# Kernel optimization log

Hardware: AMD Instinct MI355X
Metric: run time of the kernel (lower is better)

The kernel has to match this reference:

```python
import math
import jax, jax.numpy as jnp
import numpy as np

N_HEADS = 12


def _rel_to_abs(x):
    # x: [b, h, L, 2L-1] relative logits -> [b, h, L, L] absolute-position scores
    b, h, L, _ = x.shape
    x = jnp.pad(x, ((0, 0), (0, 0), (0, 0), (0, 1)))           # [b,h,L,2L]
    xf = x.reshape(b, h, L * 2 * L)
    xf = jnp.pad(xf, ((0, 0), (0, 0), (0, L - 1)))
    return xf.reshape(b, h, L + 1, 2 * L - 1)[:, :, :L, L - 1:]


def _abs_to_rel(x):
    # x: [b, h, L, L] attention weights -> [b, h, L, 2L-1] relative-position weights
    b, h, L, _ = x.shape
    x = jnp.pad(x, ((0, 0), (0, 0), (0, 0), (0, L - 1)))        # [b,h,L,2L-1]
    xf = x.reshape(b, h, L * (2 * L - 1))
    xf = jnp.pad(xf, ((0, 0), (0, 0), (L, 0)))
    return xf.reshape(b, h, L, 2 * L)[:, :, :, 1:]


def _get_relative_embeddings(emb, length):
    # emb: [n_rel, 2*window+1, k] -> [n_rel, 2*length-1, k]
    window = (emb.shape[1] - 1) // 2
    pad_len = max(length - (window + 1), 0)
    start = max(window + 1 - length, 0)
    if pad_len > 0:
        emb = jnp.pad(emb, ((0, 0), (pad_len, pad_len), (0, 0)))
    return emb[:, start:start + 2 * length - 1]


def setup_inputs() -> dict:
    key = jax.random.key(0)
    ks = jax.random.split(key, 8)
    B, C, T, H = 4, 768, 1024, N_HEADS
    K = C // H
    W = 10
    xavier = math.sqrt(2.0 / (C + C))          # xavier_uniform std analogue
    rel_std = K ** (-0.5)
    return {
        "x": jax.random.normal(ks[0], (B, C, T), jnp.float32),
        "c": jax.random.normal(ks[1], (B, C, T), jnp.float32),
        "Wq": jax.random.normal(ks[2], (C, C), jnp.float32) * xavier,
        "bq": jnp.zeros((C,), jnp.float32),
        "Wk": jax.random.normal(ks[3], (C, C), jnp.float32) * xavier,
        "bk": jnp.zeros((C,), jnp.float32),
        "Wv": jax.random.normal(ks[4], (C, C), jnp.float32) * xavier,
        "bv": jnp.zeros((C,), jnp.float32),
        "Wo": jax.random.normal(ks[5], (C, C), jnp.float32) * xavier,
        "bo": jnp.zeros((C,), jnp.float32),
        "emb_rel_k": jax.random.normal(ks[6], (1, 2 * W + 1, K), jnp.float32) * rel_std,
        "emb_rel_v": jax.random.normal(ks[7], (1, 2 * W + 1, K), jnp.float32) * rel_std,
    }


def reference(x, c, Wq, bq, Wk, bk, Wv, bv, Wo, bo, emb_rel_k, emb_rel_v):
    B, C, T = x.shape
    H = N_HEADS
    K = C // H

    def proj(W_, b_, inp):  # Conv1d(kernel=1) == channel-wise linear
        return jnp.einsum('oi,bit->bot', W_, inp) + b_[None, :, None]

    # [B,C,T] -> [B,H,T,K]
    q = proj(Wq, bq, x).reshape(B, H, K, T).transpose(0, 1, 3, 2)
    k = proj(Wk, bk, c).reshape(B, H, K, T).transpose(0, 1, 3, 2)
    v = proj(Wv, bv, c).reshape(B, H, K, T).transpose(0, 1, 3, 2)

    qs = q * (1.0 / math.sqrt(K))
    scores = jnp.einsum('bhtd,bhsd->bhts', qs, k)               # [B,H,T,T]

    # relative key logits via skewing trick
    rel_k = _get_relative_embeddings(emb_rel_k, T)              # [1,2T-1,K]
    rel_logits = jnp.einsum('bhtd,md->bhtm', qs, rel_k[0])      # [B,H,T,2T-1]
    scores = scores + _rel_to_abs(rel_logits)

    # proximal bias: -log(1 + |i - j|)
    r = jnp.arange(T, dtype=scores.dtype)
    scores = scores - jnp.log1p(jnp.abs(r[None, :] - r[:, None]))[None, None]

    p = jax.nn.softmax(scores, axis=-1)
    out = jnp.einsum('bhts,bhsd->bhtd', p, v)                   # [B,H,T,K]

    # relative value contribution
    rel_v = _get_relative_embeddings(emb_rel_v, T)              # [1,2T-1,K]
    out = out + jnp.einsum('bhtm,md->bhtd', _abs_to_rel(p), rel_v[0])

    out = out.transpose(0, 1, 3, 2).reshape(B, C, T)            # [B,C,T]
    return jnp.einsum('oi,bit->bot', Wo, out) + bo[None, :, None]
```

## Files before the change

kernel.cpp:

```cpp
#include <hip/hip_runtime.h>
#include <hip/hip_bf16.h>

using bf16 = __hip_bfloat16;
typedef __attribute__((ext_vector_type(8))) short short8;
typedef __attribute__((ext_vector_type(4))) float f32x4;

static constexpr int C = 768, T = 1024, H = 12, D = 64;

__device__ __forceinline__ f32x4 mfma16(short8 a, short8 b, f32x4 c){
  return __builtin_amdgcn_mfma_f32_16x16x32_bf16(a, b, c, 0, 0, 0);
}

__device__ __forceinline__ void gload16(const void* g, void* l){
  void* gv = const_cast<void*>(g);
  __builtin_amdgcn_global_load_lds((__attribute__((address_space(1))) void*)gv,
                                   (__attribute__((address_space(3))) void*)l, 16, 0, 0);
}

__device__ __forceinline__ float b2f(short s){
  unsigned u = ((unsigned)(unsigned short)s) << 16;
  return __builtin_bit_cast(float, u);
}

__device__ __forceinline__ int cvtpk(float a, float b){
  int r;
  asm("v_cvt_pk_bf16_f32 %0, %1, %2" : "=v"(r) : "v"(a), "v"(b));
  return r;
}

union PkU { int i[4]; short8 v; };

__global__ __launch_bounds__(256) void prep_kernel(const float* __restrict__ xin,
    const float* __restrict__ cin, const float* __restrict__ Wq,
    const float* __restrict__ Wk, const float* __restrict__ Wv,
    const float* __restrict__ Wo, bf16* __restrict__ xo, bf16* __restrict__ co,
    bf16* __restrict__ wq, bf16* __restrict__ wk, bf16* __restrict__ wv,
    bf16* __restrict__ wo){
  const int z = blockIdx.z;
  if (z < 8){
    __shared__ float tile[64][65];
    const int b = z & 3, which = z >> 2;
    const float* in = which ? cin : xin;
    bf16* out = which ? co : xo;
    const int t0 = blockIdx.x*64, c0 = blockIdx.y*64;
    const int u = threadIdx.x & 63, r0 = threadIdx.x >> 6;
    const float* ip = in + ((size_t)b*C + c0)*T + t0;
    #pragma unroll
    for (int i = r0; i < 64; i += 4) tile[i][u] = ip[(size_t)i*T + u];
    __syncthreads();
    bf16* op = out + ((size_t)b*T + t0)*C + c0;
    #pragma unroll
    for (int j = r0; j < 64; j += 4) op[(size_t)j*C + u] = (bf16)tile[u][j];
  } else {
    const int chunk = (z - 8)*192 + blockIdx.y*16 + blockIdx.x;
    const int m = chunk / 576;
    const int off = (chunk % 576)*1024 + threadIdx.x*4;
    const float* in = m==0 ? Wq : m==1 ? Wk : m==2 ? Wv : Wo;
    bf16* out = m==0 ? wq : m==1 ? wk : m==2 ? wv : wo;
    float4 v = *(const float4*)(in + off);
    out[off+0] = (bf16)v.x; out[off+1] = (bf16)v.y;
    out[off+2] = (bf16)v.z; out[off+3] = (bf16)v.w;
  }
}

__global__ __launch_bounds__(256,3) void gemm_qkv(const bf16* __restrict__ xb,
    const bf16* __restrict__ cb, const bf16* __restrict__ wq, const bf16* __restrict__ wk,
    const bf16* __restrict__ wv, const float* __restrict__ bq, const float* __restrict__ bk,
    const float* __restrict__ bv, bf16* __restrict__ qout, bf16* __restrict__ kout,
    bf16* __restrict__ vout){
  const int tid = threadIdx.x, lane = tid & 63, w = tid >> 6;
  const int wr = w >> 1, wc = w & 1, g = lane >> 4, cl = lane & 15;
  const int bz = blockIdx.y, b = bz & 3, mode = bz >> 2;
  const int lb = blockIdx.x;
  int m0, n0;
  if (mode == 2){ m0 = (lb >> 3)*128; n0 = (lb & 7)*128; }
  else          { m0 = (lb / 6)*128;  n0 = (lb % 6)*128; }
  const bf16* A  = (mode==0) ? xb + (size_t)b*T*C : (mode==1) ? cb + (size_t)b*T*C : wv;
  const bf16* Bp = (mode==2) ? cb + (size_t)b*T*C : (mode==0) ? wq : wk;
  const float* bias = (mode==0) ? bq : (mode==1) ? bk : bv;
  const float scale = (mode==0) ? 0.125f*1.44269504088896f : 1.0f;
  __shared__ bf16 lA[128*64], lB[128*64];
  f32x4 acc[4][4] = {};
  const bf16* Ars = A  + (size_t)m0*768;
  const bf16* Brs = Bp + (size_t)n0*768;
  for (int k0 = 0; k0 < 768; k0 += 64){
    __syncthreads();
    #pragma unroll
    for (int rr = 0; rr < 4; ++rr){
      const int u = rr*256 + tid;
      const int row = u >> 3, cc = u & 7;
      const int src = row*768 + k0 + ((cc ^ (row & 7))*8);
      gload16(Ars + src, &lA[(size_t)u*8]);
      gload16(Brs + src, &lB[(size_t)u*8]);
    }
    __syncthreads();
    #pragma unroll
    for (int kh = 0; kh < 2; ++kh){
      short8 af[4], bfr[4];
      #pragma unroll
      for (int mi = 0; mi < 4; ++mi){
        const int row = wr*64 + mi*16 + cl;
        af[mi] = *(const short8*)&lA[row*64 + (((g + kh*4) ^ (row & 7))*8)];
      }
      #pragma unroll
      for (int ni = 0; ni < 4; ++ni){
        const int row = wc*64 + ni*16 + cl;
        bfr[ni] = *(const short8*)&lB[row*64 + (((g + kh*4) ^ (row & 7))*8)];
      }
      __builtin_amdgcn_s_setprio(1);
      #pragma unroll
      for (int mi = 0; mi < 4; ++mi)
        #pragma unroll
        for (int ni = 0; ni < 4; ++ni)
          acc[mi][ni] = mfma16(af[mi], bfr[ni], acc[mi][ni]);
      __builtin_amdgcn_s_setprio(0);
    }
  }
  #pragma unroll
  for (int mi = 0; mi < 4; ++mi){
    const int mB = m0 + wr*64 + mi*16 + g*4;
    #pragma unroll
    for (int ni = 0; ni < 4; ++ni){
      const int n = n0 + wc*64 + ni*16 + cl;
      #pragma unroll
      for (int r = 0; r < 4; ++r){
        const int m = mB + r;
        float v = acc[mi][ni][r];
        if (mode <= 1){
          v = (v + bias[n]) * scale;
          bf16* outp = mode ? kout : qout;
          outp[(size_t)b*(H*T*D) + (size_t)(n >> 6)*(T*D) + (size_t)m*D + (n & 63)] = (bf16)v;
        } else {
          v += bias[m];
          vout[(size_t)b*(C*T) + (size_t)m*T + n] = (bf16)v;
        }
      }
    }
  }
}

__global__ __launch_bounds__(256,3) void gemm_o(const bf16* __restrict__ wo,
                                                const bf16* __restrict__ attn,
                                                const float* __restrict__ bias,
                                                float* __restrict__ outp){
  const int tid = threadIdx.x, lane = tid & 63, w = tid >> 6;
  const int wr = w >> 1, wc = w & 1, g = lane >> 4, cl = lane & 15;
  const int b = blockIdx.z;
  const int m0 = blockIdx.x*128, n0 = blockIdx.y*128;
  __shared__ bf16 lA[128*64], lB[128*64];
  f32x4 acc[4][4] = {};
  const bf16* Ars = wo + (size_t)m0*768;
  const bf16* Brs = attn + (size_t)b*T*C + (size_t)n0*768;
  for (int k0 = 0; k0 < 768; k0 += 64){
    __syncthreads();
    #pragma unroll
    for (int rr = 0; rr < 4; ++rr){
      const int u = rr*256 + tid;
      const int row = u >> 3, cc = u & 7;
      const int src = row*768 + k0 + ((cc ^ (row & 7))*8);
      gload16(Ars + src, &lA[(size_t)u*8]);
      gload16(Brs + src, &lB[(size_t)u*8]);
    }
    __syncthreads();
    #pragma unroll
    for (int kh = 0; kh < 2; ++kh){
      short8 af[4], bfr[4];
      #pragma unroll
      for (int mi = 0; mi < 4; ++mi){
        const int row = wr*64 + mi*16 + cl;
        af[mi] = *(const short8*)&lA[row*64 + (((g + kh*4) ^ (row & 7))*8)];
      }
      #pragma unroll
      for (int ni = 0; ni < 4; ++ni){
        const int row = wc*64 + ni*16 + cl;
        bfr[ni] = *(const short8*)&lB[row*64 + (((g + kh*4) ^ (row & 7))*8)];
      }
      __builtin_amdgcn_s_setprio(1);
      #pragma unroll
      for (int mi = 0; mi < 4; ++mi)
        #pragma unroll
        for (int ni = 0; ni < 4; ++ni)
          acc[mi][ni] = mfma16(af[mi], bfr[ni], acc[mi][ni]);
      __builtin_amdgcn_s_setprio(0);
    }
  }
  #pragma unroll
  for (int mi = 0; mi < 4; ++mi){
    const int mB = m0 + wr*64 + mi*16 + g*4;
    #pragma unroll
    for (int ni = 0; ni < 4; ++ni){
      const int n = n0 + wc*64 + ni*16 + cl;
      #pragma unroll
      for (int r = 0; r < 4; ++r){
        const int m = mB + r;
        outp[(size_t)b*(C*T) + (size_t)m*T + n] = acc[mi][ni][r] + bias[m];
      }
    }
  }
}

__global__ __launch_bounds__(256,3) void attn_kernel(const bf16* __restrict__ qws,
                                                     const bf16* __restrict__ kws,
                                                     const bf16* __restrict__ vws,
                                                     bf16* __restrict__ aws,
                                                     const float* __restrict__ relk,
                                                     const float* __restrict__ relv){
  const int tid = threadIdx.x, lane = tid & 63, w = tid >> 6;
  const int g = lane >> 4, cl = lane & 15;
  const int i0 = blockIdx.x*64, bh = blockIdx.y;
  const int b = bh / H, h = bh % H;
  const int ql = w*16 + cl;
  const int qt = i0 + ql;

  __shared__ __align__(16) char smem[40960];
  bf16*  lKV   = (bf16*)smem;
  float* bandS = (float*)(smem + 32768);
  bf16*  relkD = (bf16*)(smem + 38144);
  bf16*  lEmb32 = lKV + 4096;
  bf16*  lEV    = lKV;
  bf16*  lQ     = lKV + 3*4096;

  const bf16* qg = qws + ((size_t)bh*T + i0)*D;
  const bf16* kg = kws + (size_t)bh*T*D;
  const bf16* vg = vws + ((size_t)b*C + h*D)*T;

  int kOff[2], vOff[2], qOff[2], dst[2];
  #pragma unroll
  for (int r = 0; r < 2; ++r){
    const int u = r*256 + tid, L = u >> 3, cc = u & 7;
    const int sc8 = (cc ^ (L & 7))*8;
    const int sig = (((L>>4)&1)<<5) | (((L>>2)&3)<<3) | (((L>>5)&1)<<2) | (L&3);
    kOff[r] = sig*64 + sc8;
    vOff[r] = L*T + sc8;
    qOff[r] = L*64 + sc8;
    dst[r]  = u*8;
  }

  #pragma unroll
  for (int r = 0; r < 2; ++r){
    gload16(qg + qOff[r], &lQ[dst[r]]);
    gload16(kg + kOff[r], &lKV[dst[r]]);
    gload16(vg + vOff[r], &lKV[2*4096 + dst[r]]);
  }
  for (int idx = tid; idx < 2048; idx += 256){
    const int row = idx >> 6, col = idx & 63;
    const float v = (row < 21) ? relk[idx] : 0.0f;
    lEmb32[row*64 + (((col >> 3) ^ (row & 7))*8) + (col & 7)] = (bf16)v;
  }
  __syncthreads();

  const short8 aq0 = *(const short8*)&lQ[ql*64 + ((g ^ (ql & 7))*8)];
  const short8 aq1 = *(const short8*)&lQ[ql*64 + (((g + 4) ^ (ql & 7))*8)];

  #pragma unroll
  for (int ni2 = 0; ni2 < 2; ++ni2){
    const int row = ni2*16 + cl;
    short8 e0 = *(const short8*)&lEmb32[row*64 + ((g ^ (row & 7))*8)];
    short8 e1 = *(const short8*)&lEmb32[row*64 + (((g + 4) ^ (row & 7))*8)];
    f32x4 rk = {};
    rk = mfma16(e0, aq0, rk);
    rk = mfma16(e1, aq1, rk);
    #pragma unroll
    for (int rr = 0; rr < 4; ++rr){
      const int ridx = ni2*16 + 4*g + rr;
      if (ridx < 21) relkD[ql*22 + ridx] = (bf16)rk[rr];
    }
  }
  __syncthreads();

  float mreg = -1e30f, lreg = 0.f;
  f32x4 o[4] = {};
  const int koffA[4] = {8*g, 32 + 8*g, 4 + 8*g, 36 + 8*g};

  for (int jt = 0; jt < 16; ++jt){
    const int j0 = jt*64, cur = jt & 1, nxt = cur ^ 1;
    if (jt < 15){
      const int jn = j0 + 64;
      #pragma unroll
      for (int r = 0; r < 2; ++r){
        gload16(kg + jn*64 + kOff[r], &lKV[nxt*4096 + dst[r]]);
        gload16(vg + jn + vOff[r],    &lKV[(2 + nxt)*4096 + dst[r]]);
      }
      asm volatile("s_waitcnt vmcnt(4)" ::: "memory");
    } else {
      asm volatile("s_waitcnt vmcnt(0)" ::: "memory");
    }
    asm volatile("s_barrier" ::: "memory");

    const bf16* Kc = lKV + cur*4096;
    const bf16* Vc = lKV + (2 + cur)*4096;

    f32x4 s[4] = {};
    __builtin_amdgcn_s_setprio(1);
    #pragma unroll
    for (int ni = 0; ni < 4; ++ni){
      const int row = ni*16 + cl;
      short8 k0f = *(const short8*)&Kc[row*64 + ((g ^ (row & 7))*8)];
      s[ni] = mfma16(k0f, aq0, s[ni]);
      short8 k1f = *(const short8*)&Kc[row*64 + (((g + 4) ^ (row & 7))*8)];
      s[ni] = mfma16(k1f, aq1, s[ni]);
    }
    __builtin_amdgcn_s_setprio(0);

    const int dj = j0 - i0;
    if (dj == 0 || dj == 64 || dj == -64){
      #pragma unroll
      for (int ni = 0; ni < 4; ++ni){
        const int ibase = j0 + koffA[ni] - qt;
        #pragma unroll
        for (int r = 0; r < 4; ++r){
          const int dd = ibase + r;
          float v = s[ni][r] - __log2f(fabsf((float)dd) + 1.0f);
          if ((unsigned)(dd + 10) <= 20u){
            v += b2f(*(const short*)&relkD[ql*22 + dd + 10]);
            bandS[ql*21 + dd + 10] = v;
          }
          s[ni][r] = v;
        }
      }
    } else {
      #pragma unroll
      for (int ni = 0; ni < 4; ++ni){
        const float fb = (float)(j0 + koffA[ni] - qt);
        #pragma unroll
        for (int r = 0; r < 4; ++r)
          s[ni][r] -= __log2f(fabsf(fb + (float)r) + 1.0f);
      }
    }

    float m0 = fmaxf(fmaxf(s[0][0], s[0][1]), fmaxf(s[0][2], s[0][3]));
    float m1 = fmaxf(fmaxf(s[1][0], s[1][1]), fmaxf(s[1][2], s[1][3]));
    float m2 = fmaxf(fmaxf(s[2][0], s[2][1]), fmaxf(s[2][2], s[2][3]));
    float m3 = fmaxf(fmaxf(s[3][0], s[3][1]), fmaxf(s[3][2], s[3][3]));
    float mx = fmaxf(fmaxf(m0, m1), fmaxf(m2, m3));
    mx = fmaxf(mx, __shfl_xor(mx, 16));
    mx = fmaxf(mx, __shfl_xor(mx, 32));
    const float mn = fmaxf(mreg, mx);
    if (!__all(mn == mreg)){
      const float sc = __builtin_amdgcn_exp2f(mreg - mn);
      lreg *= sc;
      #pragma unroll
      for (int di = 0; di < 4; ++di)
        #pragma unroll
        for (int r = 0; r < 4; ++r) o[di][r] *= sc;
      mreg = mn;
    }
    float rs = 0.f;
    #pragma unroll
    for (int ni = 0; ni < 4; ++ni)
      #pragma unroll
      for (int r = 0; r < 4; ++r){
        float p = __builtin_amdgcn_exp2f(s[ni][r] - mreg);
        s[ni][r] = p; rs += p;
      }
    rs += __shfl_xor(rs, 16);
    rs += __shfl_xor(rs, 32);
    lreg += rs;

    PkU bf0, bf1;
    bf0.i[0] = cvtpk(s[0][0], s[0][1]); bf0.i[1] = cvtpk(s[0][2], s[0][3]);
    bf0.i[2] = cvtpk(s[2][0], s[2][1]); bf0.i[3] = cvtpk(s[2][2], s[2][3]);
    bf1.i[0] = cvtpk(s[1][0], s[1][1]); bf1.i[1] = cvtpk(s[1][2], s[1][3]);
    bf1.i[2] = cvtpk(s[3][0], s[3][1]); bf1.i[3] = cvtpk(s[3][2], s[3][3]);

    __builtin_amdgcn_s_setprio(1);
    #pragma unroll
    for (int di = 0; di < 4; ++di){
      const int vrow = di*16 + cl;
      short8 a0 = *(const short8*)&Vc[vrow*64 + ((g ^ (vrow & 7))*8)];
      o[di] = mfma16(a0, bf0.v, o[di]);
      short8 a1 = *(const short8*)&Vc[vrow*64 + (((g + 4) ^ (vrow & 7))*8)];
      o[di] = mfma16(a1, bf1.v, o[di]);
    }
    __builtin_amdgcn_s_setprio(0);
    asm volatile("s_barrier" ::: "memory");
  }

  for (int idx = tid; idx < 2048; idx += 256){
    const int d = idx >> 5, c = idx & 31;
    const float v = (c < 21) ? relv[c*64 + d] : 0.0f;
    lEV[d*32 + (((c >> 3) ^ ((d >> 2) & 3))*8) + (c & 7)] = (bf16)v;
  }
  __syncthreads();

  const float invl = 1.0f / lreg;
  float pb[8];
  #pragma unroll
  for (int e = 0; e < 8; ++e){
    const int ddi = 8*g + e;
    float pv = 0.f;
    if (ddi < 21){
      const int j = qt + ddi - 10;
      if (j >= 0 && j < T)
        pv = __builtin_amdgcn_exp2f(bandS[ql*21 + ddi] - mreg) * invl;
    }
    pb[e] = pv;
  }
  PkU bfE;
  bfE.i[0] = cvtpk(pb[0], pb[1]); bfE.i[1] = cvtpk(pb[2], pb[3]);
  bfE.i[2] = cvtpk(pb[4], pb[5]); bfE.i[3] = cvtpk(pb[6], pb[7]);

  bf16* outp = aws + (size_t)(b*T + qt)*C + h*64;
  #pragma unroll
  for (int di = 0; di < 4; ++di){
    const int arow = di*16 + cl;
    short8 aE = *(const short8*)&lEV[arow*32 + ((g ^ ((arow >> 2) & 3))*8)];
    f32x4 z = {};
    f32x4 ba = mfma16(aE, bfE.v, z);
    const int p0 = cvtpk(o[di][0]*invl + ba[0], o[di][1]*invl + ba[1]);
    const int p1 = cvtpk(o[di][2]*invl + ba[2], o[di][3]*invl + ba[3]);
    *(int2*)(outp + di*16 + 4*g) = make_int2(p0, p1);
  }
}

extern "C" void kernel_launch(void* const* d_in, const int* in_sizes, int n_in,
                              void* d_out, int out_size, void* d_ws, size_t ws_size,
                              hipStream_t stream){
  const float* x    = (const float*)d_in[0];
  const float* cin  = (const float*)d_in[1];
  const float* Wq   = (const float*)d_in[2];
  const float* bq   = (const float*)d_in[3];
  const float* Wk   = (const float*)d_in[4];
  const float* bk   = (const float*)d_in[5];
  const float* Wv   = (const float*)d_in[6];
  const float* bv   = (const float*)d_in[7];
  const float* Wo   = (const float*)d_in[8];
  const float* bo   = (const float*)d_in[9];
  const float* relk = (const float*)d_in[10];
  const float* relv = (const float*)d_in[11];

  char* ws = (char*)d_ws;
  constexpr size_t SZ_W = (size_t)768*768*2;
  constexpr size_t SZ_T = (size_t)4*1024*768*2;
  bf16* wq  = (bf16*)(ws + 0*SZ_W);
  bf16* wk  = (bf16*)(ws + 1*SZ_W);
  bf16* wv  = (bf16*)(ws + 2*SZ_W);
  bf16* wo  = (bf16*)(ws + 3*SZ_W);
  bf16* xb  = (bf16*)(ws + 4*SZ_W);
  bf16* cb  = (bf16*)(ws + 4*SZ_W + 1*SZ_T);
  bf16* qws = (bf16*)(ws + 4*SZ_W + 2*SZ_T);
  bf16* kws = (bf16*)(ws + 4*SZ_W + 3*SZ_T);
  bf16* vws = (bf16*)(ws + 4*SZ_W + 4*SZ_T);
  bf16* attn = xb;

  prep_kernel<<<dim3(16,12,20), 256, 0, stream>>>(x, cin, Wq, Wk, Wv, Wo,
                                                  xb, cb, wq, wk, wv, wo);
  gemm_qkv<<<dim3(48,12), 256, 0, stream>>>(xb, cb, wq, wk, wv, bq, bk, bv, qws, kws, vws);
  attn_kernel<<<dim3(16,48), 256, 0, stream>>>(qws, kws, vws, attn, relk, relv);
  gemm_o<<<dim3(6,8,4), 256, 0, stream>>>(wo, attn, bo, (float*)d_out);
}
```

Before: 98.10 us.

## Software-pipeline attention loop: overlap QK^T of next tile with softmax-PV of previous

Restructures the flash-attention loop so each iteration computes QK^T for tile t while doing softmax and PV for tile t-1, with K and V loads staggered by one tile in separate double buffers. The aim is to hide MFMA latency behind the exp/log VALU work and to spread memory traffic across iterations. It also adds a lazy rescale that skips the running-max update unless the new max exceeds the old by more than 8 (log2 units). This raises register pressure (two score arrays) and moves Q/embedding staging into the V buffers.

Measured after the change: 119.4 us. 21.7% more time.

```diff
diff --git a/kernel.cpp b/kernel.cpp
--- a/kernel.cpp
+++ b/kernel.cpp
@@ -213,12 +213,15 @@
   const int qt = i0 + ql;
 
   __shared__ __align__(16) char smem[40960];
-  bf16*  lKV   = (bf16*)smem;
+  bf16*  kb0   = (bf16*)smem;
+  bf16*  kb1   = (bf16*)(smem + 8192);
+  bf16*  vb0   = (bf16*)(smem + 16384);
+  bf16*  vb1   = (bf16*)(smem + 24576);
   float* bandS = (float*)(smem + 32768);
   bf16*  relkD = (bf16*)(smem + 38144);
-  bf16*  lEmb32 = lKV + 4096;
-  bf16*  lEV    = lKV;
-  bf16*  lQ     = lKV + 3*4096;
+  bf16*  lQ     = vb0;
+  bf16*  lEmb32 = vb1;
+  bf16*  lEV    = kb0;
 
   const bf16* qg = qws + ((size_t)bh*T + i0)*D;
   const bf16* kg = kws + (size_t)bh*T*D;
@@ -239,8 +242,7 @@
   #pragma unroll
   for (int r = 0; r < 2; ++r){
     gload16(qg + qOff[r], &lQ[dst[r]]);
-    gload16(kg + kOff[r], &lKV[dst[r]]);
-    gload16(vg + vOff[r], &lKV[2*4096 + dst[r]]);
+    gload16(kg + kOff[r], &kb0[dst[r]]);
   }
   for (int idx = tid; idx < 2048; idx += 256){
     const int row = idx >> 6, col = idx & 63;
@@ -270,73 +272,46 @@
 
   float mreg = -1e30f, lreg = 0.f;
   f32x4 o[4] = {};
+  f32x4 sA[4], sB[4];
   const int koffA[4] = {8*g, 32 + 8*g, 4 + 8*g, 36 + 8*g};
-
-  for (int jt = 0; jt < 16; ++jt){
-    const int j0 = jt*64, cur = jt & 1, nxt = cur ^ 1;
-    if (jt < 15){
-      const int jn = j0 + 64;
-      #pragma unroll
-      for (int r = 0; r < 2; ++r){
-        gload16(kg + jn*64 + kOff[r], &lKV[nxt*4096 + dst[r]]);
-        gload16(vg + jn + vOff[r],    &lKV[(2 + nxt)*4096 + dst[r]]);
-      }
-      asm volatile("s_waitcnt vmcnt(4)" ::: "memory");
-    } else {
-      asm volatile("s_waitcnt vmcnt(0)" ::: "memory");
-    }
-    asm volatile("s_barrier" ::: "memory");
-
-    const bf16* Kc = lKV + cur*4096;
-    const bf16* Vc = lKV + (2 + cur)*4096;
-
-    f32x4 s[4] = {};
-    __builtin_amdgcn_s_setprio(1);
-    #pragma unroll
-    for (int ni = 0; ni < 4; ++ni){
-      const int row = ni*16 + cl;
-      short8 k0f = *(const short8*)&Kc[row*64 + ((g ^ (row & 7))*8)];
-      s[ni] = mfma16(k0f, aq0, s[ni]);
-      short8 k1f = *(const short8*)&Kc[row*64 + (((g + 4) ^ (row & 7))*8)];
-      s[ni] = mfma16(k1f, aq1, s[ni]);
-    }
-    __builtin_amdgcn_s_setprio(0);
-
-    const int dj = j0 - i0;
-    if (dj == 0 || dj == 64 || dj == -64){
+  const f32x4 z4 = {};
+
+  auto SOFTPV = [&](int tp, int vpar, f32x4 (&sP)[4]){
+    const int jp = tp*64;
+    const int djp = jp - i0;
+    if (djp == 0 || djp == 64 || djp == -64){
       #pragma unroll
       for (int ni = 0; ni < 4; ++ni){
-        const int ibase = j0 + koffA[ni] - qt;
+        const int ibase = jp + koffA[ni] - qt;
         #pragma unroll
         for (int r = 0; r < 4; ++r){
           const int dd = ibase + r;
-          float v = s[ni][r] - __log2f(fabsf((float)dd) + 1.0f);
+          float v = sP[ni][r] - __log2f(fabsf((float)dd) + 1.0f);
           if ((unsigned)(dd + 10) <= 20u){
             v += b2f(*(const short*)&relkD[ql*22 + dd + 10]);
             bandS[ql*21 + dd + 10] = v;
           }
-          s[ni][r] = v;
+          sP[ni][r] = v;
         }
       }
     } else {
       #pragma unroll
       for (int ni = 0; ni < 4; ++ni){
-        const float fb = (float)(j0 + koffA[ni] - qt);
+        const float fb = (float)(jp + koffA[ni] - qt);
         #pragma unroll
         for (int r = 0; r < 4; ++r)
-          s[ni][r] -= __log2f(fabsf(fb + (float)r) + 1.0f);
-      }
-    }
-
-    float m0 = fmaxf(fmaxf(s[0][0], s[0][1]), fmaxf(s[0][2], s[0][3]));
-    float m1 = fmaxf(fmaxf(s[1][0], s[1][1]), fmaxf(s[1][2], s[1][3]));
-    float m2 = fmaxf(fmaxf(s[2][0], s[2][1]), fmaxf(s[2][2], s[2][3]));
-    float m3 = fmaxf(fmaxf(s[3][0], s[3][1]), fmaxf(s[3][2], s[3][3]));
-    float mx = fmaxf(fmaxf(m0, m1), fmaxf(m2, m3));
+          sP[ni][r] -= __log2f(fabsf(fb + (float)r) + 1.0f);
+      }
+    }
+
+    float mx = fmaxf(fmaxf(fmaxf(sP[0][0], sP[0][1]), fmaxf(sP[0][2], sP[0][3])),
+                     fmaxf(fmaxf(sP[1][0], sP[1][1]), fmaxf(sP[1][2], sP[1][3])));
+    mx = fmaxf(mx, fmaxf(fmaxf(fmaxf(sP[2][0], sP[2][1]), fmaxf(sP[2][2], sP[2][3])),
+                         fmaxf(fmaxf(sP[3][0], sP[3][1]), fmaxf(sP[3][2], sP[3][3]))));
     mx = fmaxf(mx, __shfl_xor(mx, 16));
     mx = fmaxf(mx, __shfl_xor(mx, 32));
-    const float mn = fmaxf(mreg, mx);
-    if (!__all(mn == mreg)){
+    if (!__all(mx <= mreg + 8.0f)){
+      const float mn = fmaxf(mreg, mx);
       const float sc = __builtin_amdgcn_exp2f(mreg - mn);
       lreg *= sc;
       #pragma unroll
@@ -350,19 +325,20 @@
     for (int ni = 0; ni < 4; ++ni)
       #pragma unroll
       for (int r = 0; r < 4; ++r){
-        float p = __builtin_amdgcn_exp2f(s[ni][r] - mreg);
-        s[ni][r] = p; rs += p;
+        float p = __builtin_amdgcn_exp2f(sP[ni][r] - mreg);
+        sP[ni][r] = p; rs += p;
       }
     rs += __shfl_xor(rs, 16);
     rs += __shfl_xor(rs, 32);
     lreg += rs;
 
     PkU bf0, bf1;
-    bf0.i[0] = cvtpk(s[0][0], s[0][1]); bf0.i[1] = cvtpk(s[0][2], s[0][3]);
-    bf0.i[2] = cvtpk(s[2][0], s[2][1]); bf0.i[3] = cvtpk(s[2][2], s[2][3]);
-    bf1.i[0] = cvtpk(s[1][0], s[1][1]); bf1.i[1] = cvtpk(s[1][2], s[1][3]);
-    bf1.i[2] = cvtpk(s[3][0], s[3][1]); bf1.i[3] = cvtpk(s[3][2], s[3][3]);
-
+    bf0.i[0] = cvtpk(sP[0][0], sP[0][1]); bf0.i[1] = cvtpk(sP[0][2], sP[0][3]);
+    bf0.i[2] = cvtpk(sP[2][0], sP[2][1]); bf0.i[3] = cvtpk(sP[2][2], sP[2][3]);
+    bf1.i[0] = cvtpk(sP[1][0], sP[1][1]); bf1.i[1] = cvtpk(sP[1][2], sP[1][3]);
+    bf1.i[2] = cvtpk(sP[3][0], sP[3][1]); bf1.i[3] = cvtpk(sP[3][2], sP[3][3]);
+
+    const bf16* Vc = vpar ? vb1 : vb0;
     __builtin_amdgcn_s_setprio(1);
     #pragma unroll
     for (int di = 0; di < 4; ++di){
@@ -373,8 +349,52 @@
       o[di] = mfma16(a1, bf1.v, o[di]);
     }
     __builtin_amdgcn_s_setprio(0);
+  };
+
+  auto ITER = [&](int tt, int par, f32x4 (&sC)[4], f32x4 (&sP)[4]){
+    if (tt < 15){
+      const int jn = (tt + 1)*64;
+      bf16* kdst = par ? kb0 : kb1;
+      #pragma unroll
+      for (int r = 0; r < 2; ++r)
+        gload16(kg + jn*64 + kOff[r], &kdst[dst[r]]);
+    }
+    {
+      bf16* vdst = par ? vb1 : vb0;
+      #pragma unroll
+      for (int r = 0; r < 2; ++r)
+        gload16(vg + tt*64 + vOff[r], &vdst[dst[r]]);
+    }
+    if (tt < 15) asm volatile("s_waitcnt vmcnt(4)" ::: "memory");
+    else         asm volatile("s_waitcnt vmcnt(2)" ::: "memory");
     asm volatile("s_barrier" ::: "memory");
-  }
+
+    const bf16* Kc = par ? kb1 : kb0;
+    __builtin_amdgcn_s_setprio(1);
+    #pragma unroll
+    for (int ni = 0; ni < 4; ++ni){
+      const int row = ni*16 + cl;
+      short8 k0f = *(const short8*)&Kc[row*64 + ((g ^ (row & 7))*8)];
+      short8 k1f = *(const short8*)&Kc[row*64 + (((g + 4) ^ (row & 7))*8)];
+      f32x4 acc = z4;
+      acc = mfma16(k0f, aq0, acc);
+      acc = mfma16(k1f, aq1, acc);
+      sC[ni] = acc;
+    }
+    __builtin_amdgcn_s_setprio(0);
+
+    if (tt > 0) SOFTPV(tt - 1, par ^ 1, sP);
+
+    asm volatile("s_barrier" ::: "memory");
+  };
+
+  for (int t2 = 0; t2 < 16; t2 += 2){
+    ITER(t2,     0, sA, sB);
+    ITER(t2 + 1, 1, sB, sA);
+  }
+  asm volatile("s_waitcnt vmcnt(0)" ::: "memory");
+  asm volatile("s_barrier" ::: "memory");
+  SOFTPV(15, 1, sB);
 
   for (int idx = tid; idx < 2048; idx += 256){
     const int d = idx >> 5, c = idx & 31;
@@ -405,8 +425,7 @@
   for (int di = 0; di < 4; ++di){
     const int arow = di*16 + cl;
     short8 aE = *(const short8*)&lEV[arow*32 + ((g ^ ((arow >> 2) & 3))*8)];
-    f32x4 z = {};
-    f32x4 ba = mfma16(aE, bfE.v, z);
+    f32x4 ba = mfma16(aE, bfE.v, z4);
     const int p0 = cvtpk(o[di][0]*invl + ba[0], o[di][1]*invl + ba[1]);
     const int p1 = cvtpk(o[di][2]*invl + ba[2], o[di][3]*invl + ba[3]);
     *(int2*)(outp + di*16 + 4*g) = make_int2(p0, p1);
```
